# Performance work log

Hardware: AMD Instinct MI355X
Metric: run time of the kernel (lower is better)

Reference implementation:

```python
import jax, jax.numpy as jnp
import numpy as np

ALPHA = 1.702
LIMIT = 7.0


def setup_inputs() -> dict:
    key = jax.random.key(0)
    ks = jax.random.split(key, 7)
    B, S, H, D, E, TOPK = 2, 2048, 2048, 2048, 8, 4
    T = B * S
    hidden_states = jax.random.normal(ks[0], (B, S, H), dtype=jnp.float32)
    gate_up_proj = jax.random.normal(ks[1], (E, H, 2 * D), dtype=jnp.float32) * 0.02
    gate_up_proj_bias = jax.random.normal(ks[2], (E, 2 * D), dtype=jnp.float32) * 0.02
    down_proj = jax.random.normal(ks[3], (E, D, H), dtype=jnp.float32) * 0.02
    down_proj_bias = jax.random.normal(ks[4], (E, H), dtype=jnp.float32) * 0.02
    rw = jax.random.uniform(ks[5], (T, E), dtype=jnp.float32)
    routing_weights = rw / jnp.sum(rw, axis=-1, keepdims=True)
    router_indices = jax.random.randint(ks[6], (T, TOPK), 0, E, dtype=jnp.int64)
    return {
        "hidden_states": hidden_states,
        "gate_up_proj": gate_up_proj,
        "gate_up_proj_bias": gate_up_proj_bias,
        "down_proj": down_proj,
        "down_proj_bias": down_proj_bias,
        "routing_weights": routing_weights,
        "router_indices": router_indices,
    }


def geglu(gate_up):
    # interleaved layout: gate = [..., 0::2], up = [..., 1::2]
    gate = gate_up[..., 0::2]
    up = gate_up[..., 1::2]
    gate = jnp.minimum(gate, LIMIT)
    up = jnp.clip(up, -LIMIT, LIMIT)
    glu = gate * jax.nn.sigmoid(gate * ALPHA)
    return (up + 1.0) * glu


def reference(hidden_states, gate_up_proj, gate_up_proj_bias, down_proj,
              down_proj_bias, routing_weights, router_indices):
    B, S, H = hidden_states.shape
    x = hidden_states.reshape(-1, H)  # [T, H]
    # per-expert batched GEMM: [E, T, 2D]
    gate_up = jnp.einsum('th,ehd->etd', x, gate_up_proj) + gate_up_proj_bias[:, None, :]
    act = geglu(gate_up)  # [E, T, D]
    out = jnp.einsum('etd,edh->eth', act, down_proj) + down_proj_bias[:, None, :]
    # weight by router probs and sum over experts
    out = out * routing_weights.T[:, :, None]  # [E, T, H]
    out = jnp.sum(out, axis=0)
    return out.reshape(B, S, H)
```

## Files before the change

kernel.cpp:

```cpp
#include <hip/hip_runtime.h>
#include <hip/hip_bf16.h>

#define ALPHA 1.702f
#define GLIMIT 7.0f

typedef __attribute__((ext_vector_type(4))) float f32x4;
typedef __attribute__((ext_vector_type(8))) __bf16 bf16x8;
typedef __attribute__((ext_vector_type(8))) short short8;

typedef __attribute__((address_space(3))) unsigned int as3_uint;
typedef const __attribute__((address_space(1))) unsigned int as1_uint;

__device__ __forceinline__ void async_copy16(void* lds, const void* g) {
    __builtin_amdgcn_global_load_lds((as1_uint*)g, (as3_uint*)lds, 16, 0, 0);
}

__device__ __forceinline__ short f2bf(float f) {
    unsigned u = __float_as_uint(f);
    unsigned r = (u + 0x7fffu + ((u >> 16) & 1u)) >> 16;
    return (short)r;
}

__global__ void cvt_bf16_kernel(const float* __restrict__ src,
                                short* __restrict__ dst, int n4) {
    int i = blockIdx.x * blockDim.x + threadIdx.x;
    if (i < n4) {
        float4 v = reinterpret_cast<const float4*>(src)[i];
        short4 o;
        o.x = f2bf(v.x); o.y = f2bf(v.y); o.z = f2bf(v.z); o.w = f2bf(v.w);
        reinterpret_cast<short4*>(dst)[i] = o;
    }
}

__global__ void transpose_cvt(const float* __restrict__ src,
                              short* __restrict__ dst, int R, int C, int perm) {
    __shared__ float t[64][65];
    const int z  = blockIdx.z;
    const int c0 = blockIdx.x * 64;
    const int r0 = blockIdx.y * 64;
    const float* s = src + (size_t)z * R * C;
    short* d = dst + (size_t)z * R * C;
    const int tid = threadIdx.x;
#pragma unroll
    for (int i = 0; i < 16; ++i) {
        int idx = i * 256 + tid;
        int r = idx >> 6, c = idx & 63;
        t[r][c] = s[(size_t)(r0 + r) * C + c0 + c];
    }
    __syncthreads();
#pragma unroll
    for (int i = 0; i < 16; ++i) {
        int idx = i * 256 + tid;
        int r = idx >> 6, c = idx & 63;
        int rr = c0 + r;
        int rloc = rr & 255;
        int rp = perm ? ((rr & ~255) | ((rloc & 1) << 7) | (rloc >> 1)) : rr;
        d[(size_t)rp * R + r0 + c] = f2bf(t[c][r]);
    }
}


struct Gemm1PSrc {
    const short* A; const short* B;
    __device__ __forceinline__ const short* operator()(int t, int h) const {
        int e = t >> 5;
        size_t ko = (size_t)(t & 31) << 6;
        if (h & 2) return B + ((size_t)e << 23) + ((size_t)(h & 1) << 18) + ko;
        return A + ((size_t)(h & 1) << 18) + ko;
    }
};

struct Gemm2Src {
    const short* act; const short* wdt; size_t aoff, boff; int kh;
    __device__ __forceinline__ const short* operator()(int t, int h) const {
        int g = (kh << 7) + t;
        int e = g >> 5;
        size_t ko = (size_t)(g & 31) << 6;
        if (h & 2) return wdt + ((size_t)e << 22) + boff + ((size_t)(h & 1) << 18) + ko;
        return act + ((size_t)e << 23) + aoff + ((size_t)(h & 1) << 18) + ko;
    }
};

#define PH_BAR()  __builtin_amdgcn_s_barrier()
#define PH_LGKM() do { asm volatile("s_waitcnt lgkmcnt(0)" ::: "memory"); \
                       __builtin_amdgcn_sched_barrier(0); } while (0)
#define VMW(n)    asm volatile("s_waitcnt vmcnt(" #n ")" ::: "memory")

template <int NT, int SEG, typename Src, typename Epi>
__device__ __forceinline__ void gemm_8phase(const Src& src, char* smem,
                                            f32x4 (&acc)[8][4], const Epi& epi) {
    const int tid  = threadIdx.x;
    const int lane = tid & 63;
    const int wid  = tid >> 6;
    const int wr   = wid >> 2;
    const int wcol = wid & 3;
    const int lhi  = lane >> 4;
    const int llo  = lane & 15;

    auto stage = [&](int buf, int h, const short* g) {
        char* dst = smem + buf * 65536 + h * 16384;
        {
            int c = tid, r = c >> 3, s = (c & 7) ^ (r & 7);
            async_copy16(dst + c * 16, g + (size_t)r * 2048 + s * 8);
        }
        {
            int c = tid + 512, r = c >> 3, s = (c & 7) ^ (r & 7);
            async_copy16(dst + c * 16, g + (size_t)r * 2048 + s * 8);
        }
    };
    auto ldfrag = [&](int buf, int h, int row, int slot) {
        return *(const bf16x8*)(smem + buf * 65536 + h * 16384 + row * 128 +
                                ((slot ^ (row & 7)) << 4));
    };

    stage(0, 0, src(0, 0)); stage(0, 2, src(0, 2));
    stage(0, 3, src(0, 3)); stage(0, 1, src(0, 1));
    stage(1, 0, src(1, 0)); stage(1, 2, src(1, 2)); stage(1, 3, src(1, 3));
    VMW(8);
    PH_BAR();

    bf16x8 a[4][2], b[4][2];
#pragma unroll
    for (int n = 0; n < 2; ++n) {
        int row = wcol * 32 + n * 16 + llo;
        b[n][0] = ldfrag(0, 2, row, lhi);
        b[n][1] = ldfrag(0, 2, row, 4 + lhi);
    }

    for (int t = 0; t < NT; ++t) {
        const int cur = t & 1, nxt = cur ^ 1;
#pragma unroll
        for (int m = 0; m < 4; ++m) {
            int row = wr * 64 + m * 16 + llo;
            a[m][0] = ldfrag(cur, 0, row, lhi);
            a[m][1] = ldfrag(cur, 0, row, 4 + lhi);
        }
        if (t + 1 < NT) stage(nxt, 1, src(t + 1, 1));
        PH_BAR(); PH_LGKM();
        __builtin_amdgcn_s_setprio(1);
#pragma unroll
        for (int m = 0; m < 4; ++m)
#pragma unroll
            for (int n = 0; n < 2; ++n)
#pragma unroll
                for (int ks = 0; ks < 2; ++ks)
                    acc[m][n] = __builtin_amdgcn_mfma_f32_16x16x32_bf16(
                        a[m][ks], b[n][ks], acc[m][n], 0, 0, 0);
        __builtin_amdgcn_s_setprio(0);
        PH_BAR();
#pragma unroll
        for (int n = 0; n < 2; ++n) {
            int row = wcol * 32 + n * 16 + llo;
            b[2 + n][0] = ldfrag(cur, 3, row, lhi);
            b[2 + n][1] = ldfrag(cur, 3, row, 4 + lhi);
        }
        if (t + 2 < NT) { stage(cur, 0, src(t + 2, 0)); VMW(10); }
        else if (t + 1 < NT) { VMW(8); }
        else { VMW(0); }
        PH_BAR(); PH_LGKM();
        __builtin_amdgcn_s_setprio(1);
#pragma unroll
        for (int m = 0; m < 4; ++m)
#pragma unroll
            for (int n = 2; n < 4; ++n)
#pragma unroll
                for (int ks = 0; ks < 2; ++ks)
                    acc[m][n] = __builtin_amdgcn_mfma_f32_16x16x32_bf16(
                        a[m][ks], b[n][ks], acc[m][n], 0, 0, 0);
        __builtin_amdgcn_s_setprio(0);
        PH_BAR();
#pragma unroll
        for (int m = 0; m < 4; ++m) {
            int row = wr * 64 + m * 16 + llo;
            a[m][0] = ldfrag(cur, 1, row, lhi);
            a[m][1] = ldfrag(cur, 1, row, 4 + lhi);
        }
        if (t + 2 < NT) stage(cur, 2, src(t + 2, 2));
        PH_BAR(); PH_LGKM();
        __builtin_amdgcn_s_setprio(1);
#pragma unroll
        for (int m = 0; m < 4; ++m)
#pragma unroll
            for (int n = 0; n < 2; ++n)
#pragma unroll
                for (int ks = 0; ks < 2; ++ks)
                    acc[4 + m][n] = __builtin_amdgcn_mfma_f32_16x16x32_bf16(
                        a[m][ks], b[n][ks], acc[4 + m][n], 0, 0, 0);
        __builtin_amdgcn_s_setprio(0);
        PH_BAR();
        if (t + 2 < NT) { stage(cur, 3, src(t + 2, 3)); VMW(8); }
        else if (t + 1 < NT) { VMW(2); }
        else { VMW(0); }
        PH_BAR(); PH_LGKM();
        __builtin_amdgcn_s_setprio(1);
        if (t + 1 < NT) {
#pragma unroll
            for (int n = 0; n < 2; ++n) {
                int row = wcol * 32 + n * 16 + llo;
                b[n][0] = ldfrag(nxt, 2, row, lhi);
                b[n][1] = ldfrag(nxt, 2, row, 4 + lhi);
            }
        }
#pragma unroll
        for (int m = 0; m < 4; ++m)
#pragma unroll
            for (int n = 2; n < 4; ++n)
#pragma unroll
                for (int ks = 0; ks < 2; ++ks)
                    acc[4 + m][n] = __builtin_amdgcn_mfma_f32_16x16x32_bf16(
                        a[m][ks], b[n][ks], acc[4 + m][n], 0, 0, 0);
        __builtin_amdgcn_s_setprio(0);
        PH_BAR();
        if (((t + 1) & (SEG - 1)) == 0) {
            epi(t / SEG, acc);
            if (t + 1 < NT) {
#pragma unroll
                for (int m = 0; m < 8; ++m)
#pragma unroll
                    for (int n = 0; n < 4; ++n)
                        acc[m][n] = (f32x4){0.f, 0.f, 0.f, 0.f};
            }
        }
    }
}

__global__ __launch_bounds__(512, 2) void gemm1_8ph(
    const short* __restrict__ xb, const short* __restrict__ wgut,
    const float* __restrict__ bias, const float* __restrict__ rwp,
    short* __restrict__ act) {
    __shared__ __align__(16) char smem[131072];
    __shared__ float rws2[2048];
    __shared__ float bias2[2048];
    const int bid = blockIdx.x;
    const int xcd = bid & 7, j = bid >> 3;
    const int n0 = (((xcd << 1) + (j >> 4)) << 8);
    const int m0 = ((j & 15) << 8);
    const int tid  = threadIdx.x;
    const int lane = tid & 63;
    const int wid  = tid >> 6;
    const int wr = wid >> 2, wcol = wid & 3;
    const int lhi = lane >> 4, llo = lane & 15;

    ((float4*)rws2)[tid] = ((const float4*)(rwp + (size_t)m0 * 8))[tid];
    {
        int idx = tid << 2;
        int ei = idx >> 8, c = idx & 255;
        ((float4*)bias2)[tid] =
            *(const float4*)(bias + (size_t)ei * 4096 + n0 + c);
    }

    f32x4 acc[8][4];
#pragma unroll
    for (int m = 0; m < 8; ++m)
#pragma unroll
        for (int n = 0; n < 4; ++n) acc[m][n] = (f32x4){0.f, 0.f, 0.f, 0.f};

    Gemm1PSrc src{ xb + (size_t)m0 * 2048, wgut + (size_t)n0 * 2048 };
    const int a0 = n0 >> 1;

    auto epi = [&](int e, f32x4 (&ac)[8][4]) {
        short* acte = act + ((size_t)e << 23);
        float bg[2], bu[2];
#pragma unroll
        for (int n = 0; n < 2; ++n) {
            int acol = wcol * 32 + n * 16 + llo;
            bg[n] = bias2[(e << 8) + 2 * acol];
            bu[n] = bias2[(e << 8) + 2 * acol + 1];
        }
        PH_LGKM();
        PH_BAR();
#pragma unroll
        for (int c = 0; c < 4; ++c) {
            char* slot = smem + ((c & 1) ? 32768 : 81920);
#pragma unroll
            for (int mb = 0; mb < 2; ++mb) {
                int m = 2 * c + mb;
                int rowb = (m >> 2) * 128 + wr * 64 + (m & 3) * 16 + (lhi << 2);
#pragma unroll
                for (int n = 0; n < 2; ++n) {
                    int acol = wcol * 32 + n * 16 + llo;
#pragma unroll
                    for (int q = 0; q < 4; ++q) {
                        float g = ac[m][n][q] + bg[n];
                        float u = ac[m][n + 2][q] + bu[n];
                        g = fminf(g, GLIMIT);
                        u = fmaxf(fminf(u, GLIMIT), -GLIMIT);
                        float glu = g / (1.f + __expf(-ALPHA * g));
                        float aa = (u + 1.f) * glu * rws2[(rowb + q) * 8 + e];
                        int lrow = wr * 32 + mb * 16 + (lhi << 2) + q;
                        *(short*)(slot + lrow * 256 +
                                  (((acol << 1) ^ ((lrow & 15) << 4)))) = f2bf(aa);
                    }
                }
            }
            PH_LGKM();
            PH_BAR();
#pragma unroll
            for (int i = 0; i < 2; ++i) {
                int idx = i * 512 + tid;
                int lrow = idx >> 4, g16 = idx & 15;
                int grow = ((c >> 1) << 7) + ((lrow >> 5) << 6) +
                           (((c & 1) * 2 + ((lrow >> 4) & 1)) << 4) + (lrow & 15);
                short8 vv = *(const short8*)(slot + lrow * 256 +
                                             ((g16 ^ (lrow & 15)) << 4));
                *(short8*)(acte + (size_t)(m0 + grow) * 2048 + a0 + g16 * 8) = vv;
            }
        }
        PH_BAR();
    };
    gemm_8phase<256, 32>(src, smem, acc, epi);
}

__global__ __launch_bounds__(512, 2) void gemm2_8ph(
    const short* __restrict__ act, const short* __restrict__ wdt,
    float* __restrict__ out, float* __restrict__ part) {
    __shared__ __align__(16) char smem[131072];
    const int kh = blockIdx.z;
    int flat = blockIdx.x + (blockIdx.y << 3);
    int swz = (flat & 7) * 16 + (flat >> 3);
    const int n0 = (swz & 7) * 256;
    const int m0 = (swz >> 3) * 256;
    const int tid  = threadIdx.x;
    const int lane = tid & 63;
    const int wid  = tid >> 6;
    const int wr = wid >> 2, wcol = wid & 3;

    f32x4 acc[8][4];
#pragma unroll
    for (int m = 0; m < 8; ++m)
#pragma unroll
        for (int n = 0; n < 4; ++n) acc[m][n] = (f32x4){0.f, 0.f, 0.f, 0.f};

    Gemm2Src src{ act, wdt, (size_t)m0 * 2048, (size_t)n0 * 2048, kh };
    float* dst = (kh == 0) ? out : part;

    auto epi = [&](int, f32x4 (&ac)[8][4]) {
#pragma unroll
        for (int m = 0; m < 8; ++m) {
            int row = m0 + (m >> 2) * 128 + wr * 64 + (m & 3) * 16 + ((lane >> 4) << 2);
#pragma unroll
            for (int n = 0; n < 4; ++n) {
                int col = n0 + (n >> 1) * 128 + wcol * 32 + (n & 1) * 16 + (lane & 15);
#pragma unroll
                for (int q = 0; q < 4; ++q)
                    dst[(size_t)(row + q) * 2048 + col] = ac[m][n][q];
            }
        }
    };
    gemm_8phase<128, 128>(src, smem, acc, epi);
}

__global__ __launch_bounds__(256) void reduce_bias(
    const float* __restrict__ p1, const float* __restrict__ rw,
    const float* __restrict__ bd, float* __restrict__ out) {
    const int t = blockIdx.x;
    const int tid = threadIdx.x;
    float rwv[8];
#pragma unroll
    for (int e = 0; e < 8; ++e) rwv[e] = rw[(size_t)t * 8 + e];
    size_t base = (size_t)t * 2048;
#pragma unroll
    for (int i = 0; i < 2; ++i) {
        int h = (tid + i * 256) * 4;
        float4 o = *(const float4*)(out + base + h);
        float4 p = *(const float4*)(p1 + base + h);
        o.x += p.x; o.y += p.y; o.z += p.z; o.w += p.w;
#pragma unroll
        for (int e = 0; e < 8; ++e) {
            float4 bb = *(const float4*)(bd + e * 2048 + h);
            o.x += rwv[e] * bb.x; o.y += rwv[e] * bb.y;
            o.z += rwv[e] * bb.z; o.w += rwv[e] * bb.w;
        }
        *(float4*)(out + base + h) = o;
    }
}

extern "C" void kernel_launch(void* const* d_in, const int* in_sizes, int n_in,
                              void* d_out, int out_size, void* d_ws, size_t ws_size,
                              hipStream_t stream) {
    const float* x   = (const float*)d_in[0];
    const float* wgu = (const float*)d_in[1];
    const float* bgu = (const float*)d_in[2];
    const float* wd  = (const float*)d_in[3];
    const float* bd  = (const float*)d_in[4];
    const float* rw  = (const float*)d_in[5];
    float* out = (float*)d_out;

    char* ws = (char*)d_ws;
    short* xb   = (short*)(ws);
    short* wgut = (short*)(ws + 16777216);
    float* p1   = (float*)(ws + 16777216);
    short* wdt  = (short*)(ws + 150994944);
    short* actb = (short*)(ws + 218103808);

    cvt_bf16_kernel<<<8192, 256, 0, stream>>>(x, xb, 2097152);
    transpose_cvt<<<dim3(64, 32, 8), 256, 0, stream>>>(wgu, wgut, 2048, 4096, 1);
    transpose_cvt<<<dim3(32, 32, 8), 256, 0, stream>>>(wd, wdt, 2048, 2048, 0);
    gemm1_8ph<<<256, 512, 0, stream>>>(xb, wgut, bgu, rw, actb);
    gemm2_8ph<<<dim3(8, 16, 2), 512, 0, stream>>>(actb, wdt, out, p1);
    reduce_bias<<<4096, 256, 0, stream>>>(p1, rw, bd, out);
}
```

Before: 932.9 us.

## Double-buffer A/B fragments across MFMA phases and use nontemporal stores

New measurement: 1.030 ms. 10.4% more time.

```diff
diff --git a/kernel.cpp b/kernel.cpp
--- a/kernel.cpp
+++ b/kernel.cpp
@@ -119,62 +119,62 @@
     VMW(8);
     PH_BAR();
 
-    bf16x8 a[4][2], b[4][2];
+    bf16x8 a[4][2], a2[4][2], bb0[2][2], bb1[2][2];
+#pragma unroll
+    for (int m = 0; m < 4; ++m) {
+        int row = wr * 64 + m * 16 + llo;
+        a[m][0] = ldfrag(0, 0, row, lhi);
+        a[m][1] = ldfrag(0, 0, row, 4 + lhi);
+    }
 #pragma unroll
     for (int n = 0; n < 2; ++n) {
         int row = wcol * 32 + n * 16 + llo;
-        b[n][0] = ldfrag(0, 2, row, lhi);
-        b[n][1] = ldfrag(0, 2, row, 4 + lhi);
+        bb0[n][0] = ldfrag(0, 2, row, lhi);
+        bb0[n][1] = ldfrag(0, 2, row, 4 + lhi);
     }
 
     for (int t = 0; t < NT; ++t) {
         const int cur = t & 1, nxt = cur ^ 1;
-#pragma unroll
-        for (int m = 0; m < 4; ++m) {
-            int row = wr * 64 + m * 16 + llo;
-            a[m][0] = ldfrag(cur, 0, row, lhi);
-            a[m][1] = ldfrag(cur, 0, row, 4 + lhi);
-        }
         if (t + 1 < NT) stage(nxt, 1, src(t + 1, 1));
         PH_BAR(); PH_LGKM();
         __builtin_amdgcn_s_setprio(1);
 #pragma unroll
+        for (int n = 0; n < 2; ++n) {
+            int row = wcol * 32 + n * 16 + llo;
+            bb1[n][0] = ldfrag(cur, 3, row, lhi);
+            bb1[n][1] = ldfrag(cur, 3, row, 4 + lhi);
+        }
+#pragma unroll
         for (int m = 0; m < 4; ++m)
 #pragma unroll
             for (int n = 0; n < 2; ++n)
 #pragma unroll
                 for (int ks = 0; ks < 2; ++ks)
                     acc[m][n] = __builtin_amdgcn_mfma_f32_16x16x32_bf16(
-                        a[m][ks], b[n][ks], acc[m][n], 0, 0, 0);
+                        a[m][ks], bb0[n][ks], acc[m][n], 0, 0, 0);
         __builtin_amdgcn_s_setprio(0);
         PH_BAR();
-#pragma unroll
-        for (int n = 0; n < 2; ++n) {
-            int row = wcol * 32 + n * 16 + llo;
-            b[2 + n][0] = ldfrag(cur, 3, row, lhi);
-            b[2 + n][1] = ldfrag(cur, 3, row, 4 + lhi);
-        }
         if (t + 2 < NT) { stage(cur, 0, src(t + 2, 0)); VMW(10); }
         else if (t + 1 < NT) { VMW(8); }
         else { VMW(0); }
         PH_BAR(); PH_LGKM();
         __builtin_amdgcn_s_setprio(1);
 #pragma unroll
-        for (int m = 0; m < 4; ++m)
-#pragma unroll
-            for (int n = 2; n < 4; ++n)
-#pragma unroll
-                for (int ks = 0; ks < 2; ++ks)
-                    acc[m][n] = __builtin_amdgcn_mfma_f32_16x16x32_bf16(
-                        a[m][ks], b[n][ks], acc[m][n], 0, 0, 0);
-        __builtin_amdgcn_s_setprio(0);
-        PH_BAR();
-#pragma unroll
         for (int m = 0; m < 4; ++m) {
             int row = wr * 64 + m * 16 + llo;
-            a[m][0] = ldfrag(cur, 1, row, lhi);
-            a[m][1] = ldfrag(cur, 1, row, 4 + lhi);
-        }
+            a2[m][0] = ldfrag(cur, 1, row, lhi);
+            a2[m][1] = ldfrag(cur, 1, row, 4 + lhi);
+        }
+#pragma unroll
+        for (int m = 0; m < 4; ++m)
+#pragma unroll
+            for (int n = 0; n < 2; ++n)
+#pragma unroll
+                for (int ks = 0; ks < 2; ++ks)
+                    acc[m][2 + n] = __builtin_amdgcn_mfma_f32_16x16x32_bf16(
+                        a[m][ks], bb1[n][ks], acc[m][2 + n], 0, 0, 0);
+        __builtin_amdgcn_s_setprio(0);
+        PH_BAR();
         if (t + 2 < NT) stage(cur, 2, src(t + 2, 2));
         PH_BAR(); PH_LGKM();
         __builtin_amdgcn_s_setprio(1);
@@ -185,7 +185,7 @@
 #pragma unroll
                 for (int ks = 0; ks < 2; ++ks)
                     acc[4 + m][n] = __builtin_amdgcn_mfma_f32_16x16x32_bf16(
-                        a[m][ks], b[n][ks], acc[4 + m][n], 0, 0, 0);
+                        a2[m][ks], bb0[n][ks], acc[4 + m][n], 0, 0, 0);
         __builtin_amdgcn_s_setprio(0);
         PH_BAR();
         if (t + 2 < NT) { stage(cur, 3, src(t + 2, 3)); VMW(8); }
@@ -195,20 +195,26 @@
         __builtin_amdgcn_s_setprio(1);
         if (t + 1 < NT) {
 #pragma unroll
+            for (int m = 0; m < 4; ++m) {
+                int row = wr * 64 + m * 16 + llo;
+                a[m][0] = ldfrag(nxt, 0, row, lhi);
+                a[m][1] = ldfrag(nxt, 0, row, 4 + lhi);
+            }
+#pragma unroll
             for (int n = 0; n < 2; ++n) {
                 int row = wcol * 32 + n * 16 + llo;
-                b[n][0] = ldfrag(nxt, 2, row, lhi);
-                b[n][1] = ldfrag(nxt, 2, row, 4 + lhi);
+                bb0[n][0] = ldfrag(nxt, 2, row, lhi);
+                bb0[n][1] = ldfrag(nxt, 2, row, 4 + lhi);
             }
         }
 #pragma unroll
         for (int m = 0; m < 4; ++m)
 #pragma unroll
-            for (int n = 2; n < 4; ++n)
+            for (int n = 0; n < 2; ++n)
 #pragma unroll
                 for (int ks = 0; ks < 2; ++ks)
-                    acc[4 + m][n] = __builtin_amdgcn_mfma_f32_16x16x32_bf16(
-                        a[m][ks], b[n][ks], acc[4 + m][n], 0, 0, 0);
+                    acc[4 + m][2 + n] = __builtin_amdgcn_mfma_f32_16x16x32_bf16(
+                        a2[m][ks], bb1[n][ks], acc[4 + m][2 + n], 0, 0, 0);
         __builtin_amdgcn_s_setprio(0);
         PH_BAR();
         if (((t + 1) & (SEG - 1)) == 0) {
@@ -303,7 +309,8 @@
                            (((c & 1) * 2 + ((lrow >> 4) & 1)) << 4) + (lrow & 15);
                 short8 vv = *(const short8*)(slot + lrow * 256 +
                                              ((g16 ^ (lrow & 15)) << 4));
-                *(short8*)(acte + (size_t)(m0 + grow) * 2048 + a0 + g16 * 8) = vv;
+                __builtin_nontemporal_store(
+                    vv, (short8*)(acte + (size_t)(m0 + grow) * 2048 + a0 + g16 * 8));
             }
         }
         PH_BAR();
@@ -343,7 +350,8 @@
                 int col = n0 + (n >> 1) * 128 + wcol * 32 + (n & 1) * 16 + (lane & 15);
 #pragma unroll
                 for (int q = 0; q < 4; ++q)
-                    dst[(size_t)(row + q) * 2048 + col] = ac[m][n][q];
+                    __builtin_nontemporal_store(
+                        ac[m][n][q], &dst[(size_t)(row + q) * 2048 + col]);
             }
         }
     };
@@ -362,16 +370,15 @@
 #pragma unroll
     for (int i = 0; i < 2; ++i) {
         int h = (tid + i * 256) * 4;
-        float4 o = *(const float4*)(out + base + h);
-        float4 p = *(const float4*)(p1 + base + h);
-        o.x += p.x; o.y += p.y; o.z += p.z; o.w += p.w;
+        f32x4 o = __builtin_nontemporal_load((const f32x4*)(out + base + h));
+        f32x4 p = __builtin_nontemporal_load((const f32x4*)(p1 + base + h));
+        o += p;
 #pragma unroll
         for (int e = 0; e < 8; ++e) {
-            float4 bb = *(const float4*)(bd + e * 2048 + h);
-            o.x += rwv[e] * bb.x; o.y += rwv[e] * bb.y;
-            o.z += rwv[e] * bb.z; o.w += rwv[e] * bb.w;
-        }
-        *(float4*)(out + base + h) = o;
+            f32x4 bb = *(const f32x4*)(bd + e * 2048 + h);
+            o += rwv[e] * bb;
+        }
+        __builtin_nontemporal_store(o, (f32x4*)(out + base + h));
     }
 }
 
```
